# Performance work log

Hardware: AMD Instinct MI355X
Metric: run time of the kernel (lower is better)

The kernel has to match this reference:

```python
import jax, jax.numpy as jnp
import numpy as np

B, N, L, D = 1, 128, 256, 256   # batch, num_seqs, seq_len, msa_dim
P, H = 128, 8                   # pair_dim, num_heads
DH = D // H                     # head_dim


def setup_inputs() -> dict:
    key = jax.random.key(0)
    ks = jax.random.split(key, 7)
    msa = jax.random.normal(ks[0], (B, N, L, D), dtype=jnp.float32)
    pair = jax.random.normal(ks[1], (B, L, L, P), dtype=jnp.float32)
    mask = jax.random.randint(ks[2], (B, N, L), 0, 2) > 0  # bool key mask
    w_qkv = jax.random.normal(ks[3], (D, 3 * D), dtype=jnp.float32) * (D ** -0.5)
    w_pb = jax.random.normal(ks[4], (P, H), dtype=jnp.float32) * (P ** -0.5)
    b_pb = jnp.zeros((H,), dtype=jnp.float32)
    w_out = jax.random.normal(ks[5], (D, D), dtype=jnp.float32) * (D ** -0.5)
    b_out = jnp.zeros((D,), dtype=jnp.float32)
    return {"msa": msa, "pair": pair, "mask": mask, "w_qkv": w_qkv,
            "w_pb": w_pb, "b_pb": b_pb, "w_out": w_out, "b_out": b_out}


def reference(msa, pair, mask, w_qkv, w_pb, b_pb, w_out, b_out):
    b, n, l, d = msa.shape
    scaling = DH ** -0.5
    qkv = msa @ w_qkv                                   # [b,n,l,3d]
    qkv = qkv.reshape(b, n, l, 3, H, DH)
    q, k, v = qkv[..., 0, :, :], qkv[..., 1, :, :], qkv[..., 2, :, :]  # [b,n,l,h,dh]
    pair_bias = (pair @ w_pb + b_pb)                    # [b,l,l,h]
    pair_bias = jnp.transpose(pair_bias, (0, 3, 1, 2))  # [b,h,l,l]
    # scores: [b,n,h,l,l]
    dots = jnp.einsum('bnqhd,bnkhd->bnhqk', q, k) * scaling
    dots = dots + pair_bias[:, None]                    # broadcast over num_seqs
    dots = jnp.where(mask[:, :, None, None, :], dots, -jnp.inf)  # mask keys
    attn = jax.nn.softmax(dots, axis=-1)
    out = jnp.einsum('bnhqk,bnkhd->bnqhd', attn, v)     # [b,n,l,h,dh]
    out = out.reshape(b, n, l, d)
    return out @ w_out + b_out
```

## Files before the change

kernel.cpp:

```cpp
#include <hip/hip_runtime.h>
#include <hip/hip_bf16.h>

#define NN 128
#define LL 256
#define DD 256
#define PP 128
#define HH 8
#define DHH 32

typedef __bf16 bf16x8 __attribute__((ext_vector_type(8)));
typedef short s16x4 __attribute__((ext_vector_type(4)));
typedef short s16x8 __attribute__((ext_vector_type(8)));
typedef float f32x4 __attribute__((ext_vector_type(4)));
typedef unsigned int u32x2 __attribute__((ext_vector_type(2)));

__device__ __forceinline__ int permk(int k) {
  return (k & 0xC3) | ((k & 0x30) >> 2) | ((k & 0x0C) << 2);
}

__device__ __forceinline__ void gload_lds16(const void* g, void* l) {
  __builtin_amdgcn_global_load_lds(
      (const __attribute__((address_space(1))) void*)g,
      (__attribute__((address_space(3))) void*)l, 16, 0, 0);
}

__global__ __launch_bounds__(256) void cvt_bf16(
    const float* __restrict__ src, __hip_bfloat16* __restrict__ dst, int n) {
  for (int i = (blockIdx.x * 256 + threadIdx.x) * 4; i < n; i += gridDim.x * 1024) {
    float4 v = *(const float4*)(src + i);
    ushort4 o;
    o.x = __bfloat16_as_ushort(__float2bfloat16(v.x));
    o.y = __bfloat16_as_ushort(__float2bfloat16(v.y));
    o.z = __bfloat16_as_ushort(__float2bfloat16(v.z));
    o.w = __bfloat16_as_ushort(__float2bfloat16(v.w));
    *(ushort4*)(dst + i) = o;
  }
}

__global__ __launch_bounds__(256) void transpose_cvt(
    const float* __restrict__ src, __hip_bfloat16* __restrict__ dst,
    int K, int N) {
  __shared__ float t[32][33];
  int n0 = blockIdx.x * 32, k0 = blockIdx.y * 32;
  int tx = threadIdx.x & 31, ty = threadIdx.x >> 5;
  for (int i = 0; i < 4; ++i) {
    int ky = ty + i * 8;
    t[ky][tx] = src[(size_t)(k0 + ky) * N + n0 + tx];
  }
  __syncthreads();
  for (int i = 0; i < 4; ++i) {
    int ny = ty + i * 8;
    dst[(size_t)(n0 + ny) * K + k0 + tx] = __float2bfloat16(t[tx][ny]);
  }
}

#define MODE_I32 0
#define MODE_I8 1
#define MODE_BF16 2
#define MODE_F32 3

__global__ __launch_bounds__(256) void mask_expand(
    const unsigned char* __restrict__ mraw, float* __restrict__ mout) {
  __shared__ int s_or1, s_or2, s_or3, s_max, s_mode;
  int tid = threadIdx.x;
  if (tid == 0) { s_or1 = 0; s_or2 = 0; s_or3 = 0; s_max = 0; }
  __syncthreads();
  int or1 = 0, or2 = 0, or3 = 0, mx = 0;
  for (int j = tid; j < 4096; j += 256) {
    int b = mraw[j];
    mx = mx > b ? mx : b;
    int r = j & 3;
    if (r == 1) or1 |= b;
    else if (r == 2) or2 |= b;
    else if (r == 3) or3 |= b;
  }
  atomicOr(&s_or1, or1); atomicOr(&s_or2, or2); atomicOr(&s_or3, or3);
  atomicMax(&s_max, mx);
  __syncthreads();
  if (tid == 0) {
    int mode;
    if (s_max <= 1) mode = ((s_or1 | s_or2 | s_or3) == 0) ? MODE_I32 : MODE_I8;
    else            mode = (s_or1 != 0) ? MODE_BF16 : MODE_F32;
    s_mode = mode;
  }
  __syncthreads();
  int mode = s_mode;
  int i0 = blockIdx.x * 1024;
  for (int i = i0 + tid; i < i0 + 1024; i += 256) {
    int v;
    if (mode == MODE_I32)       v = ((const int*)mraw)[i] != 0;
    else if (mode == MODE_I8)   v = mraw[i] != 0;
    else if (mode == MODE_BF16) v = ((const unsigned short*)mraw)[i] != 0;
    else                        v = ((const unsigned int*)mraw)[i] != 0;
    mout[(i & ~255) | permk(i & 255)] = v ? 1.f : 0.f;
  }
}

#define GSTAGE(AD, BD, KS)                                                    \
  {                                                                           \
    const int k0_ = (KS) * 32;                                                \
    gload_lds16(Aptr + ((size_t)(bm * 128 + srow)) * 256 + k0_ + scc * 8,     \
                AD + (size_t)(wv * 64) * 8);                                  \
    gload_lds16(Btptr + ((size_t)(bn * 128 + srow)) * 256 + k0_ + scc * 8,    \
                BD + (size_t)(wv * 64) * 8);                                  \
    gload_lds16(Aptr + ((size_t)(bm * 128 + 64 + srow)) * 256 + k0_ + scc * 8,\
                AD + (size_t)(wv * 64 + 256) * 8);                            \
    gload_lds16(Btptr + ((size_t)(bn * 128 + 64 + srow)) * 256 + k0_ + scc * 8,\
                BD + (size_t)(wv * 64 + 256) * 8);                            \
  }

#define GPHASE(CA, CB, NA, NB, NKS, DOSTAGE)                                  \
  {                                                                           \
    if (DOSTAGE) GSTAGE(NA, NB, NKS)                                          \
    bf16x8 af[4], bfr[4];                                                     \
    _Pragma("unroll") for (int mi = 0; mi < 4; ++mi) {                        \
      int r_ = wm + mi * 16 + lr;                                             \
      af[mi] = *(const bf16x8*)&CA[r_ * 32 + (quad ^ (r_ & 3)) * 8];          \
    }                                                                         \
    _Pragma("unroll") for (int ni = 0; ni < 4; ++ni) {                        \
      int r_ = wn + ni * 16 + lr;                                             \
      bfr[ni] = *(const bf16x8*)&CB[r_ * 32 + (quad ^ (r_ & 3)) * 8];         \
    }                                                                         \
    _Pragma("unroll") for (int mi = 0; mi < 4; ++mi)                          \
      _Pragma("unroll") for (int ni = 0; ni < 4; ++ni)                        \
        acc[mi][ni] = __builtin_amdgcn_mfma_f32_16x16x32_bf16(                \
            bfr[ni], af[mi], acc[mi][ni], 0, 0, 0);                           \
  }                                                                           \
  __syncthreads();

#define GEMM_PIPELINE(APTR_, BTPTR_)                                          \
  const __hip_bfloat16* __restrict__ Aptr = (APTR_);                          \
  const __hip_bfloat16* __restrict__ Btptr = (BTPTR_);                        \
  __shared__ __align__(16) __hip_bfloat16 As0[128 * 32], As1[128 * 32];       \
  __shared__ __align__(16) __hip_bfloat16 Bs0[128 * 32], Bs1[128 * 32];       \
  int tid = threadIdx.x;                                                      \
  int lane = tid & 63, wv = tid >> 6;                                         \
  int wm = (wv >> 1) * 64, wn = (wv & 1) * 64;                                \
  int lr = lane & 15, quad = lane >> 4;                                       \
  int bm = blockIdx.x, bn = blockIdx.y;                                       \
  int srow = tid >> 2, sslot = tid & 3;                                       \
  int scc = sslot ^ (srow & 3);                                               \
  f32x4 acc[4][4];                                                            \
  for (int i = 0; i < 4; ++i)                                                 \
    for (int j = 0; j < 4; ++j) acc[i][j] = (f32x4){0.f, 0.f, 0.f, 0.f};      \
  GSTAGE(As0, Bs0, 0)                                                         \
  __syncthreads();                                                            \
  GPHASE(As0, Bs0, As1, Bs1, 1, 1)                                            \
  GPHASE(As1, Bs1, As0, Bs0, 2, 1)                                            \
  GPHASE(As0, Bs0, As1, Bs1, 3, 1)                                            \
  GPHASE(As1, Bs1, As0, Bs0, 4, 1)                                            \
  GPHASE(As0, Bs0, As1, Bs1, 5, 1)                                            \
  GPHASE(As1, Bs1, As0, Bs0, 6, 1)                                            \
  GPHASE(As0, Bs0, As1, Bs1, 7, 1)                                            \
  GPHASE(As1, Bs1, As0, Bs0, 8, 0)

__global__ __launch_bounds__(256) void qkv_gemm_mfma(
    const __hip_bfloat16* __restrict__ A,
    const __hip_bfloat16* __restrict__ Bt,
    __hip_bfloat16* __restrict__ qb,
    __hip_bfloat16* __restrict__ kb,
    __hip_bfloat16* __restrict__ vb) {
  GEMM_PIPELINE(A, Bt)
  int t = bn >> 1;
#pragma unroll
  for (int mi = 0; mi < 4; ++mi) {
    int g = bm * 128 + wm + mi * 16 + lr;
    int n = g >> 8, l = g & 255;
    int lp = permk(l);
#pragma unroll
    for (int ni = 0; ni < 4; ++ni) {
      int rem = (bn * 128 + wn + ni * 16 + quad * 4) & 255;
      int h = rem >> 5, dh0 = rem & 31;
      if (t < 2) {
        ushort4 w;
        w.x = __bfloat16_as_ushort(__float2bfloat16(acc[mi][ni][0]));
        w.y = __bfloat16_as_ushort(__float2bfloat16(acc[mi][ni][1]));
        w.z = __bfloat16_as_ushort(__float2bfloat16(acc[mi][ni][2]));
        w.w = __bfloat16_as_ushort(__float2bfloat16(acc[mi][ni][3]));
        __hip_bfloat16* dst = (t == 0 ? qb : kb);
        *(ushort4*)(dst + ((size_t)((n * HH + h) * LL + l)) * DHH + dh0) = w;
      } else {
#pragma unroll
        for (int r = 0; r < 4; ++r)
          vb[((size_t)((n * HH + h) * DHH + dh0 + r)) * LL + lp] =
              __float2bfloat16(acc[mi][ni][r]);
      }
    }
  }
}

__global__ __launch_bounds__(256) void out_gemm_mfma(
    const __hip_bfloat16* __restrict__ A,
    const __hip_bfloat16* __restrict__ Bt,
    const float* __restrict__ bout,
    float* __restrict__ C) {
  GEMM_PIPELINE(A, Bt)
#pragma unroll
  for (int mi = 0; mi < 4; ++mi) {
    int g = bm * 128 + wm + mi * 16 + lr;
#pragma unroll
    for (int ni = 0; ni < 4; ++ni) {
      int gcol0 = bn * 128 + wn + ni * 16 + quad * 4;
      float4 bo = *(const float4*)(bout + gcol0);
      float4 v;
      v.x = acc[mi][ni][0] + bo.x;
      v.y = acc[mi][ni][1] + bo.y;
      v.z = acc[mi][ni][2] + bo.z;
      v.w = acc[mi][ni][3] + bo.w;
      *(float4*)(C + (size_t)g * 256 + gcol0) = v;
    }
  }
}

__global__ __launch_bounds__(256) void pair_bias_kernel(
    const float* __restrict__ pair,
    const float* __restrict__ w_pb,
    const float* __restrict__ b_pb,
    __hip_bfloat16* __restrict__ expb) {
  __shared__ float wp[128][9];
  __shared__ float rows[32][129];
  int tid = threadIdx.x;
  for (int i = 0; i < 4; ++i) {
    int e = tid + i * 256;
    wp[e >> 3][e & 7] = w_pb[e];
  }
  int row0 = blockIdx.x * 32;
  const float* src = pair + (size_t)row0 * PP;
  for (int i = 0; i < 16; ++i) {
    int e = tid + i * 256;
    int r = e >> 7, c = e & 127;
    rows[r][c] = src[r * 128 + c];
  }
  __syncthreads();
  int h = tid >> 5, rl = tid & 31;
  float acc = b_pb[h] - 12.0f;
  for (int p = 0; p < 128; ++p)
    acc += rows[rl][p] * wp[p][h];
  int row = row0 + rl;
  int i = row >> 8, j = row & 255;
  expb[((size_t)(h * LL + i)) * LL + permk(j)] = __float2bfloat16(__expf(acc));
}

__global__ __launch_bounds__(256, 2) void attn_mfma(
    const __hip_bfloat16* __restrict__ qb,
    const __hip_bfloat16* __restrict__ kb,
    const __hip_bfloat16* __restrict__ vbt,
    const __hip_bfloat16* __restrict__ expb,
    const float* __restrict__ maskf,
    __hip_bfloat16* __restrict__ ao) {
  int bx = blockIdx.x;
  int h = bx >> 7, n = bx & 127;
  int nh = n * HH + h;
  int tid = threadIdx.x, lane = tid & 63, wv = tid >> 6;
  int lr = lane & 15, quad = lane >> 4;
  int wm = wv * 64;
  size_t base = (size_t)nh * (LL * DHH);

  const __hip_bfloat16* qp = qb + base;
  const __hip_bfloat16* kp = kb + base;
  const __hip_bfloat16* vp = vbt + base;
  const __hip_bfloat16* ep = expb + (size_t)h * LL * LL;
  const float* mrow = maskf + n * LL;

  const float cs = 0.17677669529663687f * 1.4426950408889634f;

  bf16x8 aq[4];
#pragma unroll
  for (int mi = 0; mi < 4; ++mi)
    aq[mi] = *(const bf16x8*)(qp + (size_t)(wm + mi * 16 + lr) * DHH + quad * 8);

  bf16x8 bkA[4], bkB[4];
  s16x8 avA0a, avA0b, avA1a, avA1b;
  s16x8 avB0a, avB0b, avB1a, avB1b;
  uint4 e0a, e0b, e1a, e1b, e2a, e2b, e3a, e3b;
  f32x4 mw0, mw1, mw2, mw3;

#define LOADKT(S, KT)                                                          \
  {                                                                            \
    const int j0_ = (KT) * 64;                                                 \
    _Pragma("unroll") for (int nj = 0; nj < 4; ++nj)                           \
        bk##S[nj] =                                                            \
        *(const bf16x8*)(kp + (size_t)(j0_ + nj * 16 + lr) * DHH + quad * 8);  \
    av##S##0a = *(const s16x8*)(vp + (size_t)lr * LL + j0_ + quad * 16);       \
    av##S##0b = *(const s16x8*)(vp + (size_t)lr * LL + j0_ + quad * 16 + 8);   \
    av##S##1a = *(const s16x8*)(vp + (size_t)(16 + lr) * LL + j0_ + quad * 16);\
    av##S##1b =                                                                \
        *(const s16x8*)(vp + (size_t)(16 + lr) * LL + j0_ + quad * 16 + 8);    \
  }

#define LOADEB_ALL(KT)                                                         \
  {                                                                            \
    const int j0_ = (KT) * 64;                                                 \
    e0a = *(const uint4*)(ep + (size_t)(wm + 0 + lr) * LL + j0_ + quad * 16);  \
    e0b = *(const uint4*)(ep + (size_t)(wm + 0 + lr) * LL + j0_ + quad * 16 + 8);\
    e1a = *(const uint4*)(ep + (size_t)(wm + 16 + lr) * LL + j0_ + quad * 16); \
    e1b = *(const uint4*)(ep + (size_t)(wm + 16 + lr) * LL + j0_ + quad * 16 + 8);\
    e2a = *(const uint4*)(ep + (size_t)(wm + 32 + lr) * LL + j0_ + quad * 16); \
    e2b = *(const uint4*)(ep + (size_t)(wm + 32 + lr) * LL + j0_ + quad * 16 + 8);\
    e3a = *(const uint4*)(ep + (size_t)(wm + 48 + lr) * LL + j0_ + quad * 16); \
    e3b = *(const uint4*)(ep + (size_t)(wm + 48 + lr) * LL + j0_ + quad * 16 + 8);\
  }

#define LOADMW(KT)                                                             \
  {                                                                            \
    const int j0_ = (KT) * 64;                                                 \
    mw0 = *(const f32x4*)(mrow + j0_ + quad * 16 + 0);                         \
    mw1 = *(const f32x4*)(mrow + j0_ + quad * 16 + 4);                         \
    mw2 = *(const f32x4*)(mrow + j0_ + quad * 16 + 8);                         \
    mw3 = *(const f32x4*)(mrow + j0_ + quad * 16 + 12);                        \
  }

#define NJ_STEP(C, MI, NJ, EX, EY, AV0, AV1, LO)                               \
  {                                                                            \
    f32x4 s_ = __builtin_amdgcn_mfma_f32_16x16x32_bf16(                        \
        bk##C[NJ], aq[MI], (f32x4){0.f, 0.f, 0.f, 0.f}, 0, 0, 0);              \
    float em0_ = __uint_as_float((EX) << 16) * mw##NJ[0];                      \
    float em1_ = __uint_as_float((EX) & 0xffff0000u) * mw##NJ[1];              \
    float em2_ = __uint_as_float((EY) << 16) * mw##NJ[2];                      \
    float em3_ = __uint_as_float((EY) & 0xffff0000u) * mw##NJ[3];              \
    float p0_ = exp2f(s_[0] * cs) * em0_;                                      \
    float p1_ = exp2f(s_[1] * cs) * em1_;                                      \
    float p2_ = exp2f(s_[2] * cs) * em2_;                                      \
    float p3_ = exp2f(s_[3] * cs) * em3_;                                      \
    lsum[MI] += (p0_ + p1_) + (p2_ + p3_);                                     \
    unsigned lo_ =                                                             \
        ((unsigned)__bfloat16_as_ushort(__float2bfloat16(p1_)) << 16) |        \
        (unsigned)__bfloat16_as_ushort(__float2bfloat16(p0_));                 \
    unsigned hi_ =                                                             \
        ((unsigned)__bfloat16_as_ushort(__float2bfloat16(p3_)) << 16) |        \
        (unsigned)__bfloat16_as_ushort(__float2bfloat16(p2_));                 \
    u32x2 pu_ = {lo_, hi_};                                                    \
    s16x4 pb_ = __builtin_bit_cast(s16x4, pu_);                                \
    s16x4 a0_ = __builtin_shufflevector(AV0, AV0, LO, LO + 1, LO + 2, LO + 3); \
    s16x4 a1_ = __builtin_shufflevector(AV1, AV1, LO, LO + 1, LO + 2, LO + 3); \
    o_acc[MI][0] = __builtin_amdgcn_mfma_f32_16x16x16bf16_1k(                  \
        a0_, pb_, o_acc[MI][0], 0, 0, 0);                                      \
    o_acc[MI][1] = __builtin_amdgcn_mfma_f32_16x16x16bf16_1k(                  \
        a1_, pb_, o_acc[MI][1], 0, 0, 0);                                      \
  }

#define MI_PHASE(MI, C, EA, EB_)                                               \
  {                                                                            \
    NJ_STEP(C, MI, 0, EA.x, EA.y, av##C##0a, av##C##1a, 0)                     \
    NJ_STEP(C, MI, 1, EA.z, EA.w, av##C##0a, av##C##1a, 4)                     \
    NJ_STEP(C, MI, 2, EB_.x, EB_.y, av##C##0b, av##C##1b, 0)                   \
    NJ_STEP(C, MI, 3, EB_.z, EB_.w, av##C##0b, av##C##1b, 4)                   \
  }

#define KT_PHASE(KT, C, N, LAST)                                               \
  {                                                                            \
    LOADEB_ALL(KT)                                                             \
    LOADMW(KT)                                                                 \
    if (!(LAST)) LOADKT(N, (KT) + 1)                                           \
    MI_PHASE(0, C, e0a, e0b)                                                   \
    MI_PHASE(1, C, e1a, e1b)                                                   \
    MI_PHASE(2, C, e2a, e2b)                                                   \
    MI_PHASE(3, C, e3a, e3b)                                                   \
  }

  float lsum[4] = {0.f, 0.f, 0.f, 0.f};
  f32x4 o_acc[4][2];
#pragma unroll
  for (int mi = 0; mi < 4; ++mi)
#pragma unroll
    for (int no = 0; no < 2; ++no) o_acc[mi][no] = (f32x4){0.f, 0.f, 0.f, 0.f};

  LOADKT(A, 0)

  KT_PHASE(0, A, B, 0)
  KT_PHASE(1, B, A, 0)
  KT_PHASE(2, A, B, 0)
  KT_PHASE(3, B, A, 1)

#undef LOADKT
#undef LOADEB_ALL
#undef LOADMW
#undef NJ_STEP
#undef MI_PHASE
#undef KT_PHASE

#pragma unroll
  for (int mi = 0; mi < 4; ++mi) {
    float ls = lsum[mi];
    ls += __shfl_xor(ls, 16);
    ls += __shfl_xor(ls, 32);
    float inv = (ls > 0.f) ? 1.f / ls : 0.f;
    int q = wm + mi * 16 + lr;
#pragma unroll
    for (int no = 0; no < 2; ++no) {
      f32x4 o = o_acc[mi][no];
      ushort4 w;
      w.x = __bfloat16_as_ushort(__float2bfloat16(o[0] * inv));
      w.y = __bfloat16_as_ushort(__float2bfloat16(o[1] * inv));
      w.z = __bfloat16_as_ushort(__float2bfloat16(o[2] * inv));
      w.w = __bfloat16_as_ushort(__float2bfloat16(o[3] * inv));
      *(ushort4*)(ao + (size_t)n * (LL * DD) + (size_t)q * DD +
                  h * DHH + no * 16 + quad * 4) = w;
    }
  }
}

extern "C" void kernel_launch(void* const* d_in, const int* in_sizes, int n_in,
                              void* d_out, int out_size, void* d_ws, size_t ws_size,
                              hipStream_t stream) {
  const float* msa   = (const float*)d_in[0];
  const float* pair  = (const float*)d_in[1];
  const unsigned char* mask = (const unsigned char*)d_in[2];
  const float* w_qkv = (const float*)d_in[3];
  const float* w_pb  = (const float*)d_in[4];
  const float* b_pb  = (const float*)d_in[5];
  const float* w_out = (const float*)d_in[6];
  const float* b_out = (const float*)d_in[7];
  float* out = (float*)d_out;

  char* ws = (char*)d_ws;
  __hip_bfloat16* qb      = (__hip_bfloat16*)(ws);
  __hip_bfloat16* kb      = (__hip_bfloat16*)(ws + 16777216);
  __hip_bfloat16* vb      = (__hip_bfloat16*)(ws + 33554432);
  __hip_bfloat16* msa_c   = (__hip_bfloat16*)(ws + 50331648);
  __hip_bfloat16* ao      = (__hip_bfloat16*)(ws + 50331648);
  __hip_bfloat16* expb    = (__hip_bfloat16*)(ws + 67108864);
  __hip_bfloat16* wqkv_t  = (__hip_bfloat16*)(ws + 71303168);
  __hip_bfloat16* wout_t  = (__hip_bfloat16*)(ws + 71696384);
  float*          msk     = (float*)(ws + 71827456);

  mask_expand<<<32, 256, 0, stream>>>(mask, msk);
  cvt_bf16<<<1024, 256, 0, stream>>>(msa, msa_c, NN * LL * DD);
  transpose_cvt<<<dim3(24, 8), 256, 0, stream>>>(w_qkv, wqkv_t, 256, 768);
  transpose_cvt<<<dim3(8, 8), 256, 0, stream>>>(w_out, wout_t, 256, 256);

  qkv_gemm_mfma<<<dim3(256, 6), 256, 0, stream>>>(msa_c, wqkv_t, qb, kb, vb);
  pair_bias_kernel<<<2048, 256, 0, stream>>>(pair, w_pb, b_pb, expb);
  attn_mfma<<<1024, 256, 0, stream>>>(qb, kb, vb, expb, msk, ao);
  out_gemm_mfma<<<dim3(256, 2), 256, 0, stream>>>(ao, wout_t, b_out, out);
}
```

Before: 224.5 us.

## Fold softmax scale and key mask into QKV epilogue, compute row sums via MFMA

Moves the score scale (scaling times log2 e) into the Q projection epilogue and multiplies V rows by the key mask in the QKV GEMM epilogue, so the attention inner loop no longer multiplies by the scale or the mask per element. The row sum of probabilities is now produced by an extra MFMA against a bf16 mask vector instead of per-lane adds plus cross-lane shuffles. This cuts VALU work in the hot attention loop but adds one MFMA per step and rounds the mask and the scaled Q to bf16.

New measurement: 228.4 us. Within noise of the previous version (+1.7%).

```diff
diff --git a/kernel.cpp b/kernel.cpp
--- a/kernel.cpp
+++ b/kernel.cpp
@@ -13,6 +13,8 @@
 typedef short s16x8 __attribute__((ext_vector_type(8)));
 typedef float f32x4 __attribute__((ext_vector_type(4)));
 typedef unsigned int u32x2 __attribute__((ext_vector_type(2)));
+
+#define QSCALE_CS 0.2550889091487754f
 
 __device__ __forceinline__ int permk(int k) {
   return (k & 0xC3) | ((k & 0x30) >> 2) | ((k & 0x0C) << 2);
@@ -60,7 +62,7 @@
 #define MODE_F32 3
 
 __global__ __launch_bounds__(256) void mask_expand(
-    const unsigned char* __restrict__ mraw, float* __restrict__ mout) {
+    const unsigned char* __restrict__ mraw, __hip_bfloat16* __restrict__ mout) {
   __shared__ int s_or1, s_or2, s_or3, s_max, s_mode;
   int tid = threadIdx.x;
   if (tid == 0) { s_or1 = 0; s_or2 = 0; s_or3 = 0; s_max = 0; }
@@ -92,7 +94,7 @@
     else if (mode == MODE_I8)   v = mraw[i] != 0;
     else if (mode == MODE_BF16) v = ((const unsigned short*)mraw)[i] != 0;
     else                        v = ((const unsigned int*)mraw)[i] != 0;
-    mout[(i & ~255) | permk(i & 255)] = v ? 1.f : 0.f;
+    mout[(i & ~255) | permk(i & 255)] = __float2bfloat16(v ? 1.f : 0.f);
   }
 }
 
@@ -157,6 +159,7 @@
 __global__ __launch_bounds__(256) void qkv_gemm_mfma(
     const __hip_bfloat16* __restrict__ A,
     const __hip_bfloat16* __restrict__ Bt,
+    const __hip_bfloat16* __restrict__ mskb,
     __hip_bfloat16* __restrict__ qb,
     __hip_bfloat16* __restrict__ kb,
     __hip_bfloat16* __restrict__ vb) {
@@ -167,23 +170,25 @@
     int g = bm * 128 + wm + mi * 16 + lr;
     int n = g >> 8, l = g & 255;
     int lp = permk(l);
+    float vm = (t == 2) ? __bfloat162float(mskb[n * 256 + lp]) : 1.f;
+    float sc = (t == 0) ? QSCALE_CS : ((t == 2) ? vm : 1.f);
 #pragma unroll
     for (int ni = 0; ni < 4; ++ni) {
       int rem = (bn * 128 + wn + ni * 16 + quad * 4) & 255;
       int h = rem >> 5, dh0 = rem & 31;
       if (t < 2) {
         ushort4 w;
-        w.x = __bfloat16_as_ushort(__float2bfloat16(acc[mi][ni][0]));
-        w.y = __bfloat16_as_ushort(__float2bfloat16(acc[mi][ni][1]));
-        w.z = __bfloat16_as_ushort(__float2bfloat16(acc[mi][ni][2]));
-        w.w = __bfloat16_as_ushort(__float2bfloat16(acc[mi][ni][3]));
+        w.x = __bfloat16_as_ushort(__float2bfloat16(acc[mi][ni][0] * sc));
+        w.y = __bfloat16_as_ushort(__float2bfloat16(acc[mi][ni][1] * sc));
+        w.z = __bfloat16_as_ushort(__float2bfloat16(acc[mi][ni][2] * sc));
+        w.w = __bfloat16_as_ushort(__float2bfloat16(acc[mi][ni][3] * sc));
         __hip_bfloat16* dst = (t == 0 ? qb : kb);
         *(ushort4*)(dst + ((size_t)((n * HH + h) * LL + l)) * DHH + dh0) = w;
       } else {
 #pragma unroll
         for (int r = 0; r < 4; ++r)
           vb[((size_t)((n * HH + h) * DHH + dh0 + r)) * LL + lp] =
-              __float2bfloat16(acc[mi][ni][r]);
+              __float2bfloat16(acc[mi][ni][r] * sc);
       }
     }
   }
@@ -246,7 +251,7 @@
     const __hip_bfloat16* __restrict__ kb,
     const __hip_bfloat16* __restrict__ vbt,
     const __hip_bfloat16* __restrict__ expb,
-    const float* __restrict__ maskf,
+    const __hip_bfloat16* __restrict__ maskb,
     __hip_bfloat16* __restrict__ ao) {
   int bx = blockIdx.x;
   int h = bx >> 7, n = bx & 127;
@@ -260,9 +265,7 @@
   const __hip_bfloat16* kp = kb + base;
   const __hip_bfloat16* vp = vbt + base;
   const __hip_bfloat16* ep = expb + (size_t)h * LL * LL;
-  const float* mrow = maskf + n * LL;
-
-  const float cs = 0.17677669529663687f * 1.4426950408889634f;
+  const __hip_bfloat16* mrow = maskb + n * LL;
 
   bf16x8 aq[4];
 #pragma unroll
@@ -273,7 +276,7 @@
   s16x8 avA0a, avA0b, avA1a, avA1b;
   s16x8 avB0a, avB0b, avB1a, avB1b;
   uint4 e0a, e0b, e1a, e1b, e2a, e2b, e3a, e3b;
-  f32x4 mw0, mw1, mw2, mw3;
+  s16x8 mb_a, mb_b;
 
 #define LOADKT(S, KT)                                                          \
   {                                                                            \
@@ -301,28 +304,25 @@
     e3b = *(const uint4*)(ep + (size_t)(wm + 48 + lr) * LL + j0_ + quad * 16 + 8);\
   }
 
-#define LOADMW(KT)                                                             \
+#define LOADMB(KT)                                                             \
   {                                                                            \
     const int j0_ = (KT) * 64;                                                 \
-    mw0 = *(const f32x4*)(mrow + j0_ + quad * 16 + 0);                         \
-    mw1 = *(const f32x4*)(mrow + j0_ + quad * 16 + 4);                         \
-    mw2 = *(const f32x4*)(mrow + j0_ + quad * 16 + 8);                         \
-    mw3 = *(const f32x4*)(mrow + j0_ + quad * 16 + 12);                        \
-  }
-
-#define NJ_STEP(C, MI, NJ, EX, EY, AV0, AV1, LO)                               \
+    mb_a = *(const s16x8*)(mrow + j0_ + quad * 16);                            \
+    mb_b = *(const s16x8*)(mrow + j0_ + quad * 16 + 8);                        \
+  }
+
+#define NJ_STEP(C, MI, NJ, EX, EY, AV0, AV1, MB, LO)                           \
   {                                                                            \
     f32x4 s_ = __builtin_amdgcn_mfma_f32_16x16x32_bf16(                        \
         bk##C[NJ], aq[MI], (f32x4){0.f, 0.f, 0.f, 0.f}, 0, 0, 0);              \
-    float em0_ = __uint_as_float((EX) << 16) * mw##NJ[0];                      \
-    float em1_ = __uint_as_float((EX) & 0xffff0000u) * mw##NJ[1];              \
-    float em2_ = __uint_as_float((EY) << 16) * mw##NJ[2];                      \
-    float em3_ = __uint_as_float((EY) & 0xffff0000u) * mw##NJ[3];              \
-    float p0_ = exp2f(s_[0] * cs) * em0_;                                      \
-    float p1_ = exp2f(s_[1] * cs) * em1_;                                      \
-    float p2_ = exp2f(s_[2] * cs) * em2_;                                      \
-    float p3_ = exp2f(s_[3] * cs) * em3_;                                      \
-    lsum[MI] += (p0_ + p1_) + (p2_ + p3_);                                     \
+    float em0_ = __uint_as_float((EX) << 16);                                  \
+    float em1_ = __uint_as_float((EX) & 0xffff0000u);                          \
+    float em2_ = __uint_as_float((EY) << 16);                                  \
+    float em3_ = __uint_as_float((EY) & 0xffff0000u);                          \
+    float p0_ = exp2f(s_[0]) * em0_;                                           \
+    float p1_ = exp2f(s_[1]) * em1_;                                           \
+    float p2_ = exp2f(s_[2]) * em2_;                                           \
+    float p3_ = exp2f(s_[3]) * em3_;                                           \
     unsigned lo_ =                                                             \
         ((unsigned)__bfloat16_as_ushort(__float2bfloat16(p1_)) << 16) |        \
         (unsigned)__bfloat16_as_ushort(__float2bfloat16(p0_));                 \
@@ -333,24 +333,28 @@
     s16x4 pb_ = __builtin_bit_cast(s16x4, pu_);                                \
     s16x4 a0_ = __builtin_shufflevector(AV0, AV0, LO, LO + 1, LO + 2, LO + 3); \
     s16x4 a1_ = __builtin_shufflevector(AV1, AV1, LO, LO + 1, LO + 2, LO + 3); \
+    s16x4 am_ = __builtin_shufflevector(MB, MB, LO, LO + 1, LO + 2, LO + 3);   \
     o_acc[MI][0] = __builtin_amdgcn_mfma_f32_16x16x16bf16_1k(                  \
         a0_, pb_, o_acc[MI][0], 0, 0, 0);                                      \
     o_acc[MI][1] = __builtin_amdgcn_mfma_f32_16x16x16bf16_1k(                  \
         a1_, pb_, o_acc[MI][1], 0, 0, 0);                                      \
+    ols_ = __builtin_amdgcn_mfma_f32_16x16x16bf16_1k(am_, pb_, ols_, 0, 0, 0); \
   }
 
 #define MI_PHASE(MI, C, EA, EB_)                                               \
   {                                                                            \
-    NJ_STEP(C, MI, 0, EA.x, EA.y, av##C##0a, av##C##1a, 0)                     \
-    NJ_STEP(C, MI, 1, EA.z, EA.w, av##C##0a, av##C##1a, 4)                     \
-    NJ_STEP(C, MI, 2, EB_.x, EB_.y, av##C##0b, av##C##1b, 0)                   \
-    NJ_STEP(C, MI, 3, EB_.z, EB_.w, av##C##0b, av##C##1b, 4)                   \
+    f32x4 ols_ = (f32x4){0.f, 0.f, 0.f, 0.f};                                  \
+    NJ_STEP(C, MI, 0, EA.x, EA.y, av##C##0a, av##C##1a, mb_a, 0)               \
+    NJ_STEP(C, MI, 1, EA.z, EA.w, av##C##0a, av##C##1a, mb_a, 4)               \
+    NJ_STEP(C, MI, 2, EB_.x, EB_.y, av##C##0b, av##C##1b, mb_b, 0)             \
+    NJ_STEP(C, MI, 3, EB_.z, EB_.w, av##C##0b, av##C##1b, mb_b, 4)             \
+    lsum[MI] += ols_[0];                                                       \
   }
 
 #define KT_PHASE(KT, C, N, LAST)                                               \
   {                                                                            \
     LOADEB_ALL(KT)                                                             \
-    LOADMW(KT)                                                                 \
+    LOADMB(KT)                                                                 \
     if (!(LAST)) LOADKT(N, (KT) + 1)                                           \
     MI_PHASE(0, C, e0a, e0b)                                                   \
     MI_PHASE(1, C, e1a, e1b)                                                   \
@@ -374,7 +378,7 @@
 
 #undef LOADKT
 #undef LOADEB_ALL
-#undef LOADMW
+#undef LOADMB
 #undef NJ_STEP
 #undef MI_PHASE
 #undef KT_PHASE
@@ -382,8 +386,6 @@
 #pragma unroll
   for (int mi = 0; mi < 4; ++mi) {
     float ls = lsum[mi];
-    ls += __shfl_xor(ls, 16);
-    ls += __shfl_xor(ls, 32);
     float inv = (ls > 0.f) ? 1.f / ls : 0.f;
     int q = wm + mi * 16 + lr;
 #pragma unroll
@@ -422,14 +424,14 @@
   __hip_bfloat16* expb    = (__hip_bfloat16*)(ws + 67108864);
   __hip_bfloat16* wqkv_t  = (__hip_bfloat16*)(ws + 71303168);
   __hip_bfloat16* wout_t  = (__hip_bfloat16*)(ws + 71696384);
-  float*          msk     = (float*)(ws + 71827456);
+  __hip_bfloat16* msk     = (__hip_bfloat16*)(ws + 71827456);
 
   mask_expand<<<32, 256, 0, stream>>>(mask, msk);
   cvt_bf16<<<1024, 256, 0, stream>>>(msa, msa_c, NN * LL * DD);
   transpose_cvt<<<dim3(24, 8), 256, 0, stream>>>(w_qkv, wqkv_t, 256, 768);
   transpose_cvt<<<dim3(8, 8), 256, 0, stream>>>(w_out, wout_t, 256, 256);
 
-  qkv_gemm_mfma<<<dim3(256, 6), 256, 0, stream>>>(msa_c, wqkv_t, qb, kb, vb);
+  qkv_gemm_mfma<<<dim3(256, 6), 256, 0, stream>>>(msa_c, wqkv_t, msk, qb, kb, vb);
   pair_bias_kernel<<<2048, 256, 0, stream>>>(pair, w_pb, b_pb, expb);
   attn_mfma<<<1024, 256, 0, stream>>>(qb, kb, vb, expb, msk, ao);
   out_gemm_mfma<<<dim3(256, 2), 256, 0, stream>>>(ao, wout_t, b_out, out);
```
